# Kernel optimization log

Hardware: AMD Instinct MI355X
Metric: run time of the kernel (lower is better)

Reference implementation:

```python
import jax, jax.numpy as jnp
import numpy as np

N = 50000      # nodes
E = 800000     # edges (avg degree 16)
IN = 128       # in_channels
OUT = 200      # out_channels


def setup_inputs() -> dict:
    key = jax.random.key(0)
    ks = jax.random.split(key, 12)
    x = jax.random.normal(ks[0], (N, IN), dtype=jnp.float32)
    src = jax.random.randint(ks[1], (E,), 0, N, dtype=jnp.int32)
    off = jax.random.randint(ks[2], (E,), 1, N, dtype=jnp.int32)
    dst = (src + off) % N  # guarantees no self-loops (PyG ChebConv removes them)
    edge_index = jnp.stack([src, dst])
    edge_weight = jax.random.uniform(ks[3], (E,), dtype=jnp.float32) + 0.1
    s = 0.05
    # scale_1 (K=1): one weight; scale_2 (K=2): two; scale_3 (K=3): three. Biases per scale.
    return {
        "x": x,
        "edge_index": edge_index,
        "edge_weight": edge_weight,
        "w1_0": jax.random.normal(ks[4], (IN, OUT), dtype=jnp.float32) * s,
        "b1": jnp.zeros((OUT,), dtype=jnp.float32),
        "w2_0": jax.random.normal(ks[5], (IN, OUT), dtype=jnp.float32) * s,
        "w2_1": jax.random.normal(ks[6], (IN, OUT), dtype=jnp.float32) * s,
        "b2": jnp.zeros((OUT,), dtype=jnp.float32),
        "w3_0": jax.random.normal(ks[7], (IN, OUT), dtype=jnp.float32) * s,
        "w3_1": jax.random.normal(ks[8], (IN, OUT), dtype=jnp.float32) * s,
        "w3_2": jax.random.normal(ks[9], (IN, OUT), dtype=jnp.float32) * s,
        "b3": jnp.zeros((OUT,), dtype=jnp.float32),
    }


def _cheb_norm(edge_index, edge_weight, num_nodes):
    # PyG ChebConv.__norm__ with normalization='sym', lambda_max=2.0:
    # L = I - D^{-1/2} A D^{-1/2}; Lhat = 2L/lambda_max - I = -D^{-1/2} A D^{-1/2}
    # (self-loop weights become exactly 0, so we can drop them)
    row, col = edge_index[0], edge_index[1]
    deg = jax.ops.segment_sum(edge_weight, row, num_segments=num_nodes)
    dis = jnp.where(deg > 0, jax.lax.rsqrt(deg), 0.0)
    return -dis[row] * edge_weight * dis[col]


def _propagate(h, src, dst, norm, num_nodes):
    # out[i] = sum_{(j->i) in E} norm_e * h[j]
    return jax.ops.segment_sum(norm[:, None] * h[src], dst, num_segments=num_nodes)


def reference(x, edge_index, edge_weight, w1_0, b1, w2_0, w2_1, b2, w3_0, w3_1, w3_2, b3):
    num_nodes = x.shape[0]
    src, dst = edge_index[0], edge_index[1]
    norm = _cheb_norm(edge_index, edge_weight, num_nodes)
    # Chebyshev recursion (shared across the three scales; identical math):
    tx0 = x                                              # T_0(L) x
    tx1 = _propagate(tx0, src, dst, norm, num_nodes)     # T_1(L) x = Lhat x
    tx2 = 2.0 * _propagate(tx1, src, dst, norm, num_nodes) - tx0  # T_2(L) x
    s1 = tx0 @ w1_0 + b1
    s2 = tx0 @ w2_0 + tx1 @ w2_1 + b2
    s3 = tx0 @ w3_0 + tx1 @ w3_1 + tx2 @ w3_2 + b3
    return (s1, s2, s3)
```

## Files before the change

### kernel.cpp

```cpp
#include <hip/hip_runtime.h>

#define IN 128
#define OUT 200
#define NT 13
#define MT 64
#define RANGES 8
#define REPLICAS 64
#define RBMAX 6272
#define CSTRIDE 64

typedef __bf16 bf16x8 __attribute__((ext_vector_type(8)));
typedef float f32x4 __attribute__((ext_vector_type(4)));
typedef unsigned short ushort;
typedef ushort ushort8 __attribute__((ext_vector_type(8)));
typedef unsigned int uint;

__device__ inline ushort f2bf(float f) {
  uint b = __float_as_uint(f);
  return (ushort)((b + 0x7FFFu + ((b >> 16) & 1u)) >> 16);
}
__device__ inline float bf_lo(uint v) { return __uint_as_float(v << 16); }
__device__ inline float bf_hi(uint v) { return __uint_as_float(v & 0xFFFF0000u); }

__device__ inline size_t pk_idx(int row, int ch) {
  int rt = row >> 4, lr = row & 15, kk = ch >> 5, hi = (ch & 31) >> 3;
  return ((size_t)(rt * 4 + kk) * 64 + hi * 16 + lr) * 8 + (ch & 7);
}

__device__ inline void gload16(const void* g, void* l) {
  __builtin_amdgcn_global_load_lds(
      (const __attribute__((address_space(1))) void*)g,
      (__attribute__((address_space(3))) void*)l, 16, 0, 0);
}


__global__ __launch_bounds__(256) void k_hist(
    const int* __restrict__ src, const int* __restrict__ dst,
    const float* __restrict__ w, float* __restrict__ deg_part,
    int* __restrict__ cnt_part, int E, int N, int RB, int SL) {
  __shared__ float degL[RBMAX];
  __shared__ int cntL[RBMAX];
  int range = blockIdx.x / REPLICAS;
  int rep = blockIdx.x % REPLICAS;
  int base = range * RB;
  int lim = min(N - base, RB);
  for (int i = threadIdx.x; i < RB; i += 256) { degL[i] = 0.f; cntL[i] = 0; }
  __syncthreads();
  int e0 = rep * SL, e1 = min(E, e0 + SL);
  for (int e = e0 + (int)threadIdx.x; e < e1; e += 256) {
    int s = src[e], d = dst[e];
    int sl = s - base, dl = d - base;
    if ((unsigned)sl < (unsigned)lim) atomicAdd(&degL[sl], w[e]);
    if ((unsigned)dl < (unsigned)lim) atomicAdd(&cntL[dl], 1);
  }
  __syncthreads();
  for (int i = threadIdx.x; i < lim; i += 256) {
    deg_part[(size_t)rep * N + base + i] = degL[i];
    cnt_part[(size_t)rep * N + base + i] = cntL[i];
  }
}


__global__ void k_dis_red(const float* __restrict__ deg_part, int* __restrict__ cnt_part,
                          float* __restrict__ dis, int* __restrict__ cnt_tot, int n) {
  int i = blockIdx.x * 256 + threadIdx.x;
  if (i >= n) return;
  float d = 0.f;
  int run = 0;
  for (int c = 0; c < REPLICAS; ++c) {
    size_t idx = (size_t)c * n + i;
    int cv = cnt_part[idx];
    cnt_part[idx] = run;
    run += cv;
    d += deg_part[idx];
  }
  cnt_tot[i] = run;
  dis[i] = d > 0.f ? rsqrtf(d) : 0.f;
}


__global__ __launch_bounds__(256) void k_fill_cast(
    const int* __restrict__ src, const int* __restrict__ dst,
    const float* __restrict__ w, const float* __restrict__ dis,
    const int* __restrict__ pref, int2* __restrict__ csr_rec,
    int E, int N, int RB, int SL,
    const float* __restrict__ x, ushort* __restrict__ xb, ushort* __restrict__ xp,
    int cast_blocks, long totx,
    const float* __restrict__ w10, const float* __restrict__ w20,
    const float* __restrict__ w21, const float* __restrict__ w30,
    const float* __restrict__ w31, const float* __restrict__ w32,
    ushort* __restrict__ wpack) {
  __shared__ int curL[RBMAX];
  if (blockIdx.x < RANGES * REPLICAS) {
    int range = blockIdx.x / REPLICAS;
    int rep = blockIdx.x % REPLICAS;
    int base = range * RB;
    int lim = min(N - base, RB);
    for (int i = threadIdx.x; i < RB; i += 256) curL[i] = 0;
    __syncthreads();
    int e0 = rep * SL, e1 = min(E, e0 + SL);
    for (int e = e0 + (int)threadIdx.x; e < e1; e += 256) {
      int d = dst[e];
      int dl = d - base;
      if ((unsigned)dl < (unsigned)lim) {
        int s = src[e];
        int r = atomicAdd(&curL[dl], 1);
        int pos = d * CSTRIDE + pref[(size_t)rep * N + d] + r;
        float nm = -dis[s] * w[e] * dis[d];
        csr_rec[pos] = make_int2(s, __float_as_int(nm));
      }
    }
  } else {
    int cid = blockIdx.x - RANGES * REPLICAS;
    if (cid < cast_blocks) {
      long i = ((long)cid * 256 + threadIdx.x) * 8;
      if (i >= totx) return;
      float4 a = *(const float4*)&x[i];
      float4 b = *(const float4*)&x[i + 4];
      ushort8 o;
      o[0] = f2bf(a.x); o[1] = f2bf(a.y); o[2] = f2bf(a.z); o[3] = f2bf(a.w);
      o[4] = f2bf(b.x); o[5] = f2bf(b.y); o[6] = f2bf(b.z); o[7] = f2bf(b.w);
      *(ushort8*)&xb[i] = o;
      int row = (int)(i >> 7), ch = (int)(i & 127);
      *(ushort8*)&xp[pk_idx(row, ch)] = o;
    } else {
      int gid = (cid - cast_blocks) * 256 + threadIdx.x;
      int total = 6 * NT * 4 * 64;
      if (gid >= total) return;
      int lane = gid & 63;
      int f = gid >> 6;
      int kk = f & 3;
      int g2 = f >> 2;
      int m = g2 % 6;
      int t = g2 / 6;
      const float* wq = (m == 0) ? w10 : (m == 1) ? w20 : (m == 2) ? w21
                      : (m == 3) ? w30 : (m == 4) ? w31 : w32;
      int col = t * 16 + (lane & 15);
      int kbase = kk * 32 + (lane >> 4) * 8;
      ushort8 o;
#pragma unroll
      for (int j = 0; j < 8; ++j)
        o[j] = (col < OUT) ? f2bf(wq[(kbase + j) * OUT + col]) : (ushort)0;
      *(ushort8*)&wpack[(((size_t)t * 24 + m * 4 + kk) * 64 + lane) * 8] = o;
    }
  }
}


template <int MODE>
__device__ __forceinline__ void gather_body(
    int gb, const ushort* __restrict__ h, const ushort* __restrict__ xb,
    const int2* __restrict__ csr_rec, const int* __restrict__ cnt_tot,
    ushort* __restrict__ out_lin, ushort* __restrict__ out_pk, int n) {
  int node = gb * 4 + ((int)threadIdx.x >> 6);
  if (node >= n) return;
  int lane = threadIdx.x & 63;
  int ch0 = lane * 2;
  int s = node * CSTRIDE;
  int e = s + cnt_tot[node];
  float lo[8], hi[8];
#pragma unroll
  for (int q = 0; q < 8; ++q) { lo[q] = 0.f; hi[q] = 0.f; }
  int p = s;
  for (; p + 7 < e; p += 8) {
    int2 rec[8]; uint v[8];
#pragma unroll
    for (int q = 0; q < 8; ++q) rec[q] = csr_rec[p + q];
#pragma unroll
    for (int q = 0; q < 8; ++q) v[q] = *(const uint*)&h[(size_t)rec[q].x * IN + ch0];
#pragma unroll
    for (int q = 0; q < 8; ++q) {
      float nm = __int_as_float(rec[q].y);
      lo[q] = fmaf(nm, bf_lo(v[q]), lo[q]);
      hi[q] = fmaf(nm, bf_hi(v[q]), hi[q]);
    }
  }
  for (; p + 1 < e; p += 2) {
    int2 r0 = csr_rec[p], r1 = csr_rec[p + 1];
    uint v0 = *(const uint*)&h[(size_t)r0.x * IN + ch0];
    uint v1 = *(const uint*)&h[(size_t)r1.x * IN + ch0];
    float n0 = __int_as_float(r0.y), n1 = __int_as_float(r1.y);
    lo[0] = fmaf(n0, bf_lo(v0), lo[0]); hi[0] = fmaf(n0, bf_hi(v0), hi[0]);
    lo[1] = fmaf(n1, bf_lo(v1), lo[1]); hi[1] = fmaf(n1, bf_hi(v1), hi[1]);
  }
  if (p < e) {
    int2 r0 = csr_rec[p];
    float n0 = __int_as_float(r0.y);
    uint v0 = *(const uint*)&h[(size_t)r0.x * IN + ch0];
    lo[2] = fmaf(n0, bf_lo(v0), lo[2]); hi[2] = fmaf(n0, bf_hi(v0), hi[2]);
  }
  float r0 = ((lo[0] + lo[1]) + (lo[2] + lo[3])) + ((lo[4] + lo[5]) + (lo[6] + lo[7]));
  float r1 = ((hi[0] + hi[1]) + (hi[2] + hi[3])) + ((hi[4] + hi[5]) + (hi[6] + hi[7]));
  if (MODE == 1) {
    uint xv = *(const uint*)&xb[(size_t)node * IN + ch0];
    r0 = 2.f * r0 - bf_lo(xv);
    r1 = 2.f * r1 - bf_hi(xv);
  }
  uint packed = (uint)f2bf(r0) | ((uint)f2bf(r1) << 16);
  if (MODE == 0)
    *(uint*)&out_lin[(size_t)node * IN + ch0] = packed;
  *(uint*)&out_pk[pk_idx(node, ch0)] = packed;
}


template <int NM, int CH0>
__device__ __forceinline__ void gemm_direct(
    const ushort* __restrict__ m0, const ushort* __restrict__ m1,
    const ushort* __restrict__ wpack, const float* __restrict__ bias,
    float* __restrict__ outm, int n, int blk) {
  int lane = threadIdx.x & 63;
  int wave = (int)threadIdx.x >> 6;
  int row0 = blk * MT + wave * 16;
  int rt = row0 >> 4;
  const ushort* mats[2] = {m0, m1};
  bf16x8 a[NM][4];
#pragma unroll
  for (int m = 0; m < NM; ++m)
#pragma unroll
    for (int kk = 0; kk < 4; ++kk) {
      size_t fi = ((size_t)rt * 4 + kk) * 512 + (size_t)lane * 8;
      a[m][kk] = __builtin_bit_cast(bf16x8, *(const ushort8*)&mats[m][fi]);
    }
#pragma unroll
  for (int m = 0; m < NM; ++m)
#pragma unroll
    for (int kk = 0; kk < 4; ++kk)
      asm volatile("" : "+v"(a[m][kk]));

  for (int t = 0; t < NT; ++t) {
    int col = t * 16 + (lane & 15);
    bool colok = col < OUT;
    float bb = bias[colok ? col : 0];
    f32x4 acc = {bb, bb, bb, bb};
#pragma unroll
    for (int mm = 0; mm < NM; ++mm) {
      const ushort* base = wpack + (((size_t)t * 24 + CH0 + mm * 4) * 64 + lane) * 8;
      bf16x8 b0 = __builtin_bit_cast(bf16x8, *(const ushort8*)&base[0 * 512]);
      bf16x8 b1 = __builtin_bit_cast(bf16x8, *(const ushort8*)&base[1 * 512]);
      bf16x8 b2 = __builtin_bit_cast(bf16x8, *(const ushort8*)&base[2 * 512]);
      bf16x8 b3 = __builtin_bit_cast(bf16x8, *(const ushort8*)&base[3 * 512]);
      acc = __builtin_amdgcn_mfma_f32_16x16x32_bf16(a[mm][0], b0, acc, 0, 0, 0);
      acc = __builtin_amdgcn_mfma_f32_16x16x32_bf16(a[mm][1], b1, acc, 0, 0, 0);
      acc = __builtin_amdgcn_mfma_f32_16x16x32_bf16(a[mm][2], b2, acc, 0, 0, 0);
      acc = __builtin_amdgcn_mfma_f32_16x16x32_bf16(a[mm][3], b3, acc, 0, 0, 0);
    }
    if (colok) {
      int rbase = row0 + (lane >> 4) * 4;
#pragma unroll
      for (int r = 0; r < 4; ++r) {
        int ra = rbase + r;
        if (ra < n) outm[(long)ra * OUT + col] = acc[r];
      }
    }
  }
}


__global__ __launch_bounds__(256, 5) void k_g1s1(
    const ushort* __restrict__ xb, const ushort* __restrict__ xp,
    const int2* __restrict__ csr_rec, const int* __restrict__ cnt_tot,
    ushort* __restrict__ tx1b, ushort* __restrict__ t1p,
    const ushort* __restrict__ wpack, const float* __restrict__ b1v,
    float* __restrict__ out1, int n, int GB) {
  if ((int)blockIdx.x < GB)
    gemm_direct<1, 0>(xp, nullptr, wpack, b1v, out1, n, blockIdx.x);
  else
    gather_body<0>(blockIdx.x - GB, xb, xb, csr_rec, cnt_tot, tx1b, t1p, n);
}


__global__ __launch_bounds__(256, 5) void k_g2s2(
    const ushort* __restrict__ xb, const ushort* __restrict__ tx1b,
    const ushort* __restrict__ xp, const ushort* __restrict__ t1p,
    const int2* __restrict__ csr_rec, const int* __restrict__ cnt_tot,
    ushort* __restrict__ t2p,
    const ushort* __restrict__ wpack, const float* __restrict__ b2v,
    float* __restrict__ out2, int n, int GB) {
  if ((int)blockIdx.x < GB)
    gemm_direct<2, 4>(xp, t1p, wpack, b2v, out2, n, blockIdx.x);
  else
    gather_body<1>(blockIdx.x - GB, tx1b, xb, csr_rec, cnt_tot, nullptr, t2p, n);
}


__global__ __launch_bounds__(256) void k_s3(
    const ushort* __restrict__ xp, const ushort* __restrict__ t1p, const ushort* __restrict__ t2p,
    const ushort* __restrict__ wpack, const float* __restrict__ b3v,
    float* __restrict__ out3, int n) {
  __shared__ ushort bsm[2][12 * 512];
  __shared__ float st[MT][212];
  int lane = threadIdx.x & 63;
  int wave = (int)threadIdx.x >> 6;
  int blk = blockIdx.x;
  int rt = (blk * MT + wave * 16) >> 4;

  bf16x8 a[3][4];
  const ushort* mats[3] = {xp, t1p, t2p};
#pragma unroll
  for (int m = 0; m < 3; ++m)
#pragma unroll
    for (int kk = 0; kk < 4; ++kk) {
      size_t fi = ((size_t)rt * 4 + kk) * 512 + (size_t)lane * 8;
      a[m][kk] = __builtin_bit_cast(bf16x8, *(const ushort8*)&mats[m][fi]);
    }
#pragma unroll
  for (int m = 0; m < 3; ++m)
#pragma unroll
    for (int kk = 0; kk < 4; ++kk)
      asm volatile("" : "+v"(a[m][kk]));

  auto stage = [&](int t, int buf) {
    const ushort* src = wpack + ((size_t)t * 24 + 12) * 512;
#pragma unroll
    for (int j = 0; j < 3; ++j) {
      int c = wave * 3 + j;
      gload16(src + (size_t)c * 512 + (size_t)lane * 8, &bsm[buf][c * 512]);
    }
  };
  stage(0, 0);
  asm volatile("s_waitcnt vmcnt(0)" ::: "memory");
  __builtin_amdgcn_s_barrier();

  f32x4 acc[NT];
#pragma unroll
  for (int t = 0; t < NT; ++t) {
    int col = t * 16 + (lane & 15);
    float bb = b3v[min(col, OUT - 1)];
    acc[t] = (f32x4){bb, bb, bb, bb};
  }

  int cur = 0;
#pragma unroll
  for (int t = 0; t < NT; ++t) {
    if (t + 1 < NT) stage(t + 1, cur ^ 1);
    const ushort* bb_ = &bsm[cur][0];
#pragma unroll
    for (int kk = 0; kk < 4; ++kk) {
#pragma unroll
      for (int mm = 0; mm < 3; ++mm) {
        bf16x8 b = __builtin_bit_cast(bf16x8,
            *(const ushort8*)&bb_[(mm * 4 + kk) * 512 + lane * 8]);
        acc[t] = __builtin_amdgcn_mfma_f32_16x16x32_bf16(a[mm][kk], b, acc[t], 0, 0, 0);
      }
    }
    asm volatile("s_waitcnt vmcnt(0)" ::: "memory");
    __builtin_amdgcn_s_barrier();
    cur ^= 1;
  }

  int rbase = wave * 16 + (lane >> 4) * 4;
#pragma unroll
  for (int t = 0; t < NT; ++t) {
    int c = t * 16 + (lane & 15);
#pragma unroll
    for (int r = 0; r < 4; ++r) st[rbase + r][c] = acc[t][r];
  }
#pragma unroll
  for (int r = 0; r < 16; ++r) {
    int lrow = wave * 16 + r;
    long grow = (long)blk * MT + lrow;
    if (grow < n && lane < 50) {
      float4 v = *(const float4*)&st[lrow][lane * 4];
      *(float4*)&out3[grow * OUT + lane * 4] = v;
    }
  }
}


extern "C" void kernel_launch(void* const* d_in, const int* in_sizes, int n_in,
                              void* d_out, int out_size, void* d_ws, size_t ws_size,
                              hipStream_t stream) {
  const float* x   = (const float*)d_in[0];
  const int*   ei  = (const int*)d_in[1];
  const float* ew  = (const float*)d_in[2];
  const float* w10 = (const float*)d_in[3];
  const float* b1  = (const float*)d_in[4];
  const float* w20 = (const float*)d_in[5];
  const float* w21 = (const float*)d_in[6];
  const float* b2  = (const float*)d_in[7];
  const float* w30 = (const float*)d_in[8];
  const float* w31 = (const float*)d_in[9];
  const float* w32 = (const float*)d_in[10];
  const float* b3  = (const float*)d_in[11];
  float* out = (float*)d_out;

  int N = in_sizes[0] / IN;
  int E = in_sizes[2];
  const int* src = ei;
  const int* dst = ei + E;

  int mtiles = (N + MT - 1) / MT;
  size_t prow = (size_t)mtiles * MT;
  size_t pksz = prow * IN * 2;

  int RB = (N + RANGES - 1) / RANGES;
  int SL = (E + REPLICAS - 1) / REPLICAS;

  char* ws = (char*)d_ws;
  size_t off = 0;
  auto alloc = [&](size_t bytes) {
    void* p = ws + off;
    off = (off + bytes + 15) & ~(size_t)15;
    return p;
  };
  float* deg_part = (float*)alloc((size_t)REPLICAS * N * 4);
  int*   cnt_part = (int*)alloc((size_t)REPLICAS * N * 4);
  float* dis      = (float*)alloc((size_t)N * 4);
  int*   cnt_tot  = (int*)alloc((size_t)N * 4);
  int2*  csr_rec  = (int2*)alloc((size_t)N * CSTRIDE * 8);
  ushort* xb      = (ushort*)alloc((size_t)N * IN * 2);
  ushort* tx1b    = (ushort*)alloc((size_t)N * IN * 2);
  ushort* xp      = (ushort*)alloc(pksz);
  ushort* t1p     = (ushort*)alloc(pksz);
  ushort* t2p     = (ushort*)alloc(pksz);
  ushort* wpack   = (ushort*)alloc((size_t)6 * NT * 4 * 64 * 8 * 2);

  int nb = (N + 255) / 256;

  long totx = (long)N * IN;
  int cast_blocks = (int)((totx / 8 + 255) / 256);
  int wp_blocks = (6 * NT * 4 * 64 + 255) / 256;
  int HB = RANGES * REPLICAS;

  long NS = (long)N * OUT;
  float* out1 = out;
  float* out2 = out + NS;
  float* out3 = out + 2 * NS;

  int gblk = (N + 3) / 4;

  k_hist<<<HB, 256, 0, stream>>>(src, dst, ew, deg_part, cnt_part, E, N, RB, SL);
  k_dis_red<<<nb, 256, 0, stream>>>(deg_part, cnt_part, dis, cnt_tot, N);
  k_fill_cast<<<HB + cast_blocks + wp_blocks, 256, 0, stream>>>(
      src, dst, ew, dis, cnt_part, csr_rec, E, N, RB, SL,
      x, xb, xp, cast_blocks, totx, w10, w20, w21, w30, w31, w32, wpack);

  k_g1s1<<<mtiles + gblk, 256, 0, stream>>>(
      xb, xp, csr_rec, cnt_tot, tx1b, t1p, wpack, b1, out1, N, mtiles);
  k_g2s2<<<mtiles + gblk, 256, 0, stream>>>(
      xb, tx1b, xp, t1p, csr_rec, cnt_tot, t2p, wpack, b2, out2, N, mtiles);
  k_s3<<<mtiles, 256, 0, stream>>>(xp, t1p, t2p, wpack, b3, out3, N);
}
```

Measured before the change: 216.7 us.

## Fuse gathers with downstream GEMMs via LDS tiles and split scale-1 GEMM across launches

Each gather kernel now processes a 64-row tile: each wave gathers 16 nodes into an LDS tile, then feeds that tile straight into the MFMA GEMM for the next scale (tx1 into scale 2, tx2 into scale 3). This drops the separate k_s3 launch, the t2p buffer and its global round trip. The scale-1 GEMM blocks are split across the two launches. The trade-off is that each wave gathers 16 nodes serially, giving less parallelism per gather than one node per wave. The scale-3 GEMM also loses its LDS double-buffered weight staging and coalesced output stores.

```diff
diff --git a/kernel.cpp b/kernel.cpp
--- a/kernel.cpp
+++ b/kernel.cpp
@@ -25,12 +25,6 @@
 __device__ inline size_t pk_idx(int row, int ch) {
   int rt = row >> 4, lr = row & 15, kk = ch >> 5, hi = (ch & 31) >> 3;
   return ((size_t)(rt * 4 + kk) * 64 + hi * 16 + lr) * 8 + (ch & 7);
-}
-
-__device__ inline void gload16(const void* g, void* l) {
-  __builtin_amdgcn_global_load_lds(
-      (const __attribute__((address_space(1))) void*)g,
-      (__attribute__((address_space(3))) void*)l, 16, 0, 0);
 }
 
 
@@ -148,14 +142,10 @@
 
 
 template <int MODE>
-__device__ __forceinline__ void gather_body(
-    int gb, const ushort* __restrict__ h, const ushort* __restrict__ xb,
+__device__ __forceinline__ void gather_node(
+    int node, int ch0, const ushort* __restrict__ h, const ushort* __restrict__ xb,
     const int2* __restrict__ csr_rec, const int* __restrict__ cnt_tot,
-    ushort* __restrict__ out_lin, ushort* __restrict__ out_pk, int n) {
-  int node = gb * 4 + ((int)threadIdx.x >> 6);
-  if (node >= n) return;
-  int lane = threadIdx.x & 63;
-  int ch0 = lane * 2;
+    float& R0, float& R1) {
   int s = node * CSTRIDE;
   int e = s + cnt_tot[node];
   float lo[8], hi[8];
@@ -196,37 +186,15 @@
     r0 = 2.f * r0 - bf_lo(xv);
     r1 = 2.f * r1 - bf_hi(xv);
   }
-  uint packed = (uint)f2bf(r0) | ((uint)f2bf(r1) << 16);
-  if (MODE == 0)
-    *(uint*)&out_lin[(size_t)node * IN + ch0] = packed;
-  *(uint*)&out_pk[pk_idx(node, ch0)] = packed;
+  R0 = r0; R1 = r1;
 }
 
 
 template <int NM, int CH0>
-__device__ __forceinline__ void gemm_direct(
-    const ushort* __restrict__ m0, const ushort* __restrict__ m1,
-    const ushort* __restrict__ wpack, const float* __restrict__ bias,
-    float* __restrict__ outm, int n, int blk) {
-  int lane = threadIdx.x & 63;
-  int wave = (int)threadIdx.x >> 6;
-  int row0 = blk * MT + wave * 16;
-  int rt = row0 >> 4;
-  const ushort* mats[2] = {m0, m1};
-  bf16x8 a[NM][4];
-#pragma unroll
-  for (int m = 0; m < NM; ++m)
-#pragma unroll
-    for (int kk = 0; kk < 4; ++kk) {
-      size_t fi = ((size_t)rt * 4 + kk) * 512 + (size_t)lane * 8;
-      a[m][kk] = __builtin_bit_cast(bf16x8, *(const ushort8*)&mats[m][fi]);
-    }
-#pragma unroll
-  for (int m = 0; m < NM; ++m)
-#pragma unroll
-    for (int kk = 0; kk < 4; ++kk)
-      asm volatile("" : "+v"(a[m][kk]));
-
+__device__ __forceinline__ void gemm_core(
+    bf16x8 (&a)[NM][4], const ushort* __restrict__ wpack,
+    const float* __restrict__ bias, float* __restrict__ outm,
+    int row0, int n, int lane) {
   for (int t = 0; t < NT; ++t) {
     int col = t * 16 + (lane & 15);
     bool colok = col < OUT;
@@ -255,115 +223,114 @@
   }
 }
 
-
-__global__ __launch_bounds__(256, 5) void k_g1s1(
+__device__ __forceinline__ void s1_block(
+    const ushort* __restrict__ xp, const ushort* __restrict__ wpack,
+    const float* __restrict__ b1v, float* __restrict__ out1, int n, int blk) {
+  int lane = threadIdx.x & 63;
+  int wave = (int)threadIdx.x >> 6;
+  int row0 = blk * MT + wave * 16;
+  int rt = row0 >> 4;
+  bf16x8 a[1][4];
+#pragma unroll
+  for (int kk = 0; kk < 4; ++kk)
+    a[0][kk] = __builtin_bit_cast(bf16x8,
+        *(const ushort8*)&xp[((size_t)rt * 4 + kk) * 512 + (size_t)lane * 8]);
+#pragma unroll
+  for (int kk = 0; kk < 4; ++kk) asm volatile("" : "+v"(a[0][kk]));
+  gemm_core<1, 0>(a, wpack, b1v, out1, row0, n, lane);
+}
+
+
+__global__ __launch_bounds__(256, 5) void k_g1s2(
     const ushort* __restrict__ xb, const ushort* __restrict__ xp,
     const int2* __restrict__ csr_rec, const int* __restrict__ cnt_tot,
     ushort* __restrict__ tx1b, ushort* __restrict__ t1p,
-    const ushort* __restrict__ wpack, const float* __restrict__ b1v,
-    float* __restrict__ out1, int n, int GB) {
-  if ((int)blockIdx.x < GB)
-    gemm_direct<1, 0>(xp, nullptr, wpack, b1v, out1, n, blockIdx.x);
-  else
-    gather_body<0>(blockIdx.x - GB, xb, xb, csr_rec, cnt_tot, tx1b, t1p, n);
-}
-
-
-__global__ __launch_bounds__(256, 5) void k_g2s2(
+    const ushort* __restrict__ wpack,
+    const float* __restrict__ b1v, const float* __restrict__ b2v,
+    float* __restrict__ out1, float* __restrict__ out2, int n, int NF, int S1OFF) {
+  if ((int)blockIdx.x >= NF) {
+    s1_block(xp, wpack, b1v, out1, n, (int)blockIdx.x - NF + S1OFF);
+    return;
+  }
+  __shared__ ushort st[4][16][136];
+  int lane = threadIdx.x & 63;
+  int wave = (int)threadIdx.x >> 6;
+  int ch0 = lane * 2;
+  int rowbase = (int)blockIdx.x * MT + wave * 16;
+  for (int i = 0; i < 16; ++i) {
+    int node = rowbase + i;
+    uint packed = 0;
+    if (node < n) {
+      float r0, r1;
+      gather_node<0>(node, ch0, xb, nullptr, csr_rec, cnt_tot, r0, r1);
+      packed = (uint)f2bf(r0) | ((uint)f2bf(r1) << 16);
+      *(uint*)&tx1b[(size_t)node * IN + ch0] = packed;
+    }
+    *(uint*)&st[wave][i][ch0] = packed;
+  }
+  __syncthreads();
+  int rt = rowbase >> 4;
+  bf16x8 a[2][4];
+#pragma unroll
+  for (int kk = 0; kk < 4; ++kk) {
+    a[0][kk] = __builtin_bit_cast(bf16x8,
+        *(const ushort8*)&xp[((size_t)rt * 4 + kk) * 512 + (size_t)lane * 8]);
+    a[1][kk] = __builtin_bit_cast(bf16x8,
+        *(const ushort8*)&st[wave][lane & 15][kk * 32 + (lane >> 4) * 8]);
+    *(ushort8*)&t1p[((size_t)rt * 4 + kk) * 512 + (size_t)lane * 8] =
+        __builtin_bit_cast(ushort8, a[1][kk]);
+  }
+#pragma unroll
+  for (int m = 0; m < 2; ++m)
+#pragma unroll
+    for (int kk = 0; kk < 4; ++kk) asm volatile("" : "+v"(a[m][kk]));
+  gemm_core<2, 4>(a, wpack, b2v, out2, rowbase, n, lane);
+}
+
+
+__global__ __launch_bounds__(256, 5) void k_g2s3(
     const ushort* __restrict__ xb, const ushort* __restrict__ tx1b,
     const ushort* __restrict__ xp, const ushort* __restrict__ t1p,
     const int2* __restrict__ csr_rec, const int* __restrict__ cnt_tot,
-    ushort* __restrict__ t2p,
-    const ushort* __restrict__ wpack, const float* __restrict__ b2v,
-    float* __restrict__ out2, int n, int GB) {
-  if ((int)blockIdx.x < GB)
-    gemm_direct<2, 4>(xp, t1p, wpack, b2v, out2, n, blockIdx.x);
-  else
-    gather_body<1>(blockIdx.x - GB, tx1b, xb, csr_rec, cnt_tot, nullptr, t2p, n);
-}
-
-
-__global__ __launch_bounds__(256) void k_s3(
-    const ushort* __restrict__ xp, const ushort* __restrict__ t1p, const ushort* __restrict__ t2p,
-    const ushort* __restrict__ wpack, const float* __restrict__ b3v,
-    float* __restrict__ out3, int n) {
-  __shared__ ushort bsm[2][12 * 512];
-  __shared__ float st[MT][212];
+    const ushort* __restrict__ wpack,
+    const float* __restrict__ b1v, const float* __restrict__ b3v,
+    float* __restrict__ out1, float* __restrict__ out3, int n, int NF, int S1OFF) {
+  if ((int)blockIdx.x >= NF) {
+    s1_block(xp, wpack, b1v, out1, n, (int)blockIdx.x - NF + S1OFF);
+    return;
+  }
+  __shared__ ushort st[4][16][136];
   int lane = threadIdx.x & 63;
   int wave = (int)threadIdx.x >> 6;
-  int blk = blockIdx.x;
-  int rt = (blk * MT + wave * 16) >> 4;
-
+  int ch0 = lane * 2;
+  int rowbase = (int)blockIdx.x * MT + wave * 16;
+  for (int i = 0; i < 16; ++i) {
+    int node = rowbase + i;
+    uint packed = 0;
+    if (node < n) {
+      float r0, r1;
+      gather_node<1>(node, ch0, tx1b, xb, csr_rec, cnt_tot, r0, r1);
+      packed = (uint)f2bf(r0) | ((uint)f2bf(r1) << 16);
+    }
+    *(uint*)&st[wave][i][ch0] = packed;
+  }
+  __syncthreads();
+  int rt = rowbase >> 4;
   bf16x8 a[3][4];
-  const ushort* mats[3] = {xp, t1p, t2p};
+#pragma unroll
+  for (int kk = 0; kk < 4; ++kk) {
+    a[0][kk] = __builtin_bit_cast(bf16x8,
+        *(const ushort8*)&xp[((size_t)rt * 4 + kk) * 512 + (size_t)lane * 8]);
+    a[1][kk] = __builtin_bit_cast(bf16x8,
+        *(const ushort8*)&t1p[((size_t)rt * 4 + kk) * 512 + (size_t)lane * 8]);
+    a[2][kk] = __builtin_bit_cast(bf16x8,
+        *(const ushort8*)&st[wave][lane & 15][kk * 32 + (lane >> 4) * 8]);
+  }
 #pragma unroll
   for (int m = 0; m < 3; ++m)
 #pragma unroll
-    for (int kk = 0; kk < 4; ++kk) {
-      size_t fi = ((size_t)rt * 4 + kk) * 512 + (size_t)lane * 8;
-      a[m][kk] = __builtin_bit_cast(bf16x8, *(const ushort8*)&mats[m][fi]);
-    }
-#pragma unroll
-  for (int m = 0; m < 3; ++m)
-#pragma unroll
-    for (int kk = 0; kk < 4; ++kk)
-      asm volatile("" : "+v"(a[m][kk]));
-
-  auto stage = [&](int t, int buf) {
-    const ushort* src = wpack + ((size_t)t * 24 + 12) * 512;
-#pragma unroll
-    for (int j = 0; j < 3; ++j) {
-      int c = wave * 3 + j;
-      gload16(src + (size_t)c * 512 + (size_t)lane * 8, &bsm[buf][c * 512]);
-    }
-  };
-  stage(0, 0);
-  asm volatile("s_waitcnt vmcnt(0)" ::: "memory");
-  __builtin_amdgcn_s_barrier();
-
-  f32x4 acc[NT];
-#pragma unroll
-  for (int t = 0; t < NT; ++t) {
-    int col = t * 16 + (lane & 15);
-    float bb = b3v[min(col, OUT - 1)];
-    acc[t] = (f32x4){bb, bb, bb, bb};
-  }
-
-  int cur = 0;
-#pragma unroll
-  for (int t = 0; t < NT; ++t) {
-    if (t + 1 < NT) stage(t + 1, cur ^ 1);
-    const ushort* bb_ = &bsm[cur][0];
-#pragma unroll
-    for (int kk = 0; kk < 4; ++kk) {
-#pragma unroll
-      for (int mm = 0; mm < 3; ++mm) {
-        bf16x8 b = __builtin_bit_cast(bf16x8,
-            *(const ushort8*)&bb_[(mm * 4 + kk) * 512 + lane * 8]);
-        acc[t] = __builtin_amdgcn_mfma_f32_16x16x32_bf16(a[mm][kk], b, acc[t], 0, 0, 0);
-      }
-    }
-    asm volatile("s_waitcnt vmcnt(0)" ::: "memory");
-    __builtin_amdgcn_s_barrier();
-    cur ^= 1;
-  }
-
-  int rbase = wave * 16 + (lane >> 4) * 4;
-#pragma unroll
-  for (int t = 0; t < NT; ++t) {
-    int c = t * 16 + (lane & 15);
-#pragma unroll
-    for (int r = 0; r < 4; ++r) st[rbase + r][c] = acc[t][r];
-  }
-#pragma unroll
-  for (int r = 0; r < 16; ++r) {
-    int lrow = wave * 16 + r;
-    long grow = (long)blk * MT + lrow;
-    if (grow < n && lane < 50) {
-      float4 v = *(const float4*)&st[lrow][lane * 4];
-      *(float4*)&out3[grow * OUT + lane * 4] = v;
-    }
-  }
+    for (int kk = 0; kk < 4; ++kk) asm volatile("" : "+v"(a[m][kk]));
+  gemm_core<3, 12>(a, wpack, b3v, out3, rowbase, n, lane);
 }
 
 
@@ -412,7 +379,6 @@
   ushort* tx1b    = (ushort*)alloc((size_t)N * IN * 2);
   ushort* xp      = (ushort*)alloc(pksz);
   ushort* t1p     = (ushort*)alloc(pksz);
-  ushort* t2p     = (ushort*)alloc(pksz);
   ushort* wpack   = (ushort*)alloc((size_t)6 * NT * 4 * 64 * 8 * 2);
 
   int nb = (N + 255) / 256;
@@ -427,7 +393,8 @@
   float* out2 = out + NS;
   float* out3 = out + 2 * NS;
 
-  int gblk = (N + 3) / 4;
+  int s1a = mtiles / 2;
+  int s1b = mtiles - s1a;
 
   k_hist<<<HB, 256, 0, stream>>>(src, dst, ew, deg_part, cnt_part, E, N, RB, SL);
   k_dis_red<<<nb, 256, 0, stream>>>(deg_part, cnt_part, dis, cnt_tot, N);
@@ -435,9 +402,8 @@
       src, dst, ew, dis, cnt_part, csr_rec, E, N, RB, SL,
       x, xb, xp, cast_blocks, totx, w10, w20, w21, w30, w31, w32, wpack);
 
-  k_g1s1<<<mtiles + gblk, 256, 0, stream>>>(
-      xb, xp, csr_rec, cnt_tot, tx1b, t1p, wpack, b1, out1, N, mtiles);
-  k_g2s2<<<mtiles + gblk, 256, 0, stream>>>(
-      xb, tx1b, xp, t1p, csr_rec, cnt_tot, t2p, wpack, b2, out2, N, mtiles);
-  k_s3<<<mtiles, 256, 0, stream>>>(xp, t1p, t2p, wpack, b3, out3, N);
-}
+  k_g1s2<<<mtiles + s1a, 256, 0, stream>>>(
+      xb, xp, csr_rec, cnt_tot, tx1b, t1p, wpack, b1, b2, out1, out2, N, mtiles, 0);
+  k_g2s3<<<mtiles + s1b, 256, 0, stream>>>(
+      xb, tx1b, xp, t1p, csr_rec, cnt_tot, wpack, b1, b3, out1, out3, N, mtiles, s1a);
+}
```

Result: slower. 245.1 us (+13.1%).
